# Kernel optimization log

Hardware: AMD Instinct MI355X
Metric: run time of the kernel (lower is better)

The kernel has to match this reference:

```python
import jax, jax.numpy as jnp
import numpy as np

DIM = 96
GS = 8          # group_size (window side)
CS = 64         # cluster_size
TOPK = 3


def setup_inputs() -> dict:
    key = jax.random.key(0)
    ks = jax.random.split(key, 12)
    B, C, H, W = 4, DIM, 256, 256
    s = 0.02
    return {
        "x":      jax.random.normal(ks[0], (B, C, H, W), jnp.float32),
        "Wq":     jax.random.normal(ks[1], (C, C), jnp.float32) * s,
        "bq":     jnp.zeros((C,), jnp.float32),
        "Wk":     jax.random.normal(ks[2], (C, C), jnp.float32) * s,
        "bk":     jnp.zeros((C,), jnp.float32),
        "Wv":     jax.random.normal(ks[3], (C, C), jnp.float32) * s,
        "bv":     jnp.zeros((C,), jnp.float32),
        "Wp":     jax.random.normal(ks[4], (C, C), jnp.float32) * s,
        "bp":     jnp.zeros((C,), jnp.float32),
        "lepe_w": jax.random.normal(ks[5], (C, 1, 3, 3), jnp.float32) * s,
        "lepe_b": jnp.zeros((C,), jnp.float32),
    }


def _dwconv3x3(x, w, b):
    # x: [N,C,h,w], w: [C,1,3,3] depthwise
    y = jax.lax.conv_general_dilated(
        x, w, window_strides=(1, 1), padding=((1, 1), (1, 1)),
        feature_group_count=x.shape[1],
        dimension_numbers=("NCHW", "OIHW", "NCHW"))
    return y + b[None, :, None, None]


def reference(x, Wq, bq, Wk, bk, Wv, bv, Wp, bp, lepe_w, lepe_b):
    B, C, H, W = x.shape
    gh, gw = H // GS, W // GS
    N = B * gh * gw                      # total windows
    itr = N // CS                        # number of clusters
    P = GS * GS                          # tokens per window
    scale = C ** (-0.5)

    # adaptive_max_pool2d to (gh,gw) == non-overlapping max pool of stride GS
    dsx = x.reshape(B, C, gh, GS, gw, GS).max(axis=(3, 5))        # [B,C,gh,gw]
    dsx = dsx.transpose(0, 2, 3, 1).reshape(itr, CS, C)           # [itr,CS,C]

    # global window-similarity with two-stage topk (faithful to nested loop)
    sim = jnp.einsum('icd,jed->icje', dsx, dsx)                   # [itr,CS,itr,CS]
    blk_s, blk_i = jax.lax.top_k(sim, TOPK)                       # [itr,CS,itr,TOPK]
    blk_gi = blk_i + (jnp.arange(itr) * CS)[None, None, :, None]  # global indices
    cat_s = blk_s.reshape(itr, CS, itr * TOPK)
    cat_i = blk_gi.reshape(itr, CS, itr * TOPK)
    fin_s, fi = jax.lax.top_k(cat_s, TOPK)                        # [itr,CS,TOPK]
    fin_i = jnp.take_along_axis(cat_i, fi, axis=-1)
    sim_score = fin_s.reshape(N, TOPK)
    sim_index = fin_i.reshape(N, TOPK)

    # window partition: [N, P, C]
    xw = x.transpose(0, 2, 3, 1).reshape(B, gh, GS, gw, GS, C)
    xw = xw.transpose(0, 1, 3, 2, 4, 5).reshape(N, P, C)

    # weighted combination of topk neighbor windows
    w = jax.nn.softmax(sim_score, axis=-1)                        # [N,TOPK]
    neighbors = xw[sim_index]                                     # [N,TOPK,P,C]
    context = jnp.einsum('nk,nkpc->npc', w, neighbors)            # [N,P,C]

    # windowed cross attention: Q from x windows, K/V from gathered context
    q = xw @ Wq + bq
    k = context @ Wk + bk
    v = context @ Wv + bv

    # lepe: depthwise conv positional bias on x windows
    x_img = xw.transpose(0, 2, 1).reshape(N, C, GS, GS)
    lepe = _dwconv3x3(x_img, lepe_w, lepe_b).reshape(N, C, P).transpose(0, 2, 1)

    attn = jax.nn.softmax(jnp.einsum('npc,nqc->npq', q, k) * scale, axis=-1)
    out = jnp.einsum('npq,nqc->npc', attn, v) + lepe
    out = out @ Wp + bp                                           # [N,P,C]

    # reverse window partition -> [B,C,H,W]
    out = out.reshape(B, gh, gw, GS, GS, C)
    out = out.transpose(0, 5, 1, 3, 2, 4).reshape(B, C, H, W)
    return out
```

## Files before the change

kernel.cpp:

```cpp
#include <hip/hip_runtime.h>

typedef __attribute__((ext_vector_type(8))) short  short8;
typedef __attribute__((ext_vector_type(4))) float  f32x4;
typedef __attribute__((ext_vector_type(4))) unsigned int uint4v;
typedef __attribute__((ext_vector_type(2))) unsigned int uint2v;

#define NEG_INF (-3.402823466e38f)

__device__ __forceinline__ unsigned short bfbits(float f) {
    unsigned u = __builtin_bit_cast(unsigned, f);
    u += 0x7fffu + ((u >> 16) & 1u);
    return (unsigned short)(u >> 16);
}
__device__ __forceinline__ unsigned pk_bf16(float lo, float hi) {
    return (unsigned)bfbits(lo) | ((unsigned)bfbits(hi) << 16);
}
__device__ __forceinline__ float lofp(unsigned u) {
    return __builtin_bit_cast(float, u << 16);
}
__device__ __forceinline__ float hifp(unsigned u) {
    return __builtin_bit_cast(float, u & 0xffff0000u);
}

__device__ __forceinline__ void ins3(float (&tv)[3], int (&ti)[3], float v, int ci)
{
    if (v > tv[0] || (v == tv[0] && ci < ti[0])) {
        tv[2] = tv[1]; ti[2] = ti[1];
        tv[1] = tv[0]; ti[1] = ti[0];
        tv[0] = v;     ti[0] = ci;
    } else if (v > tv[1] || (v == tv[1] && ci < ti[1])) {
        tv[2] = tv[1]; ti[2] = ti[1];
        tv[1] = v;     ti[1] = ci;
    } else if (v > tv[2] || (v == tv[2] && ci < ti[2])) {
        tv[2] = v;     ti[2] = ci;
    }
}

__global__ __launch_bounds__(256) void k_pool(const float* __restrict__ x,
                                              float* __restrict__ dsxT)
{
    int gid = blockIdx.x * 256 + threadIdx.x;
    int c = gid >> 12;
    int n = gid & 4095;
    int b = n >> 10, i = (n >> 5) & 31, j = n & 31;
    const float* p = x + (((size_t)(b * 96 + c)) << 16) + i * 2048 + j * 8;
    float4 m0 = *(const float4*)p;
    float4 m1 = *(const float4*)(p + 4);
    #pragma unroll
    for (int r = 1; r < 8; ++r) {
        float4 a0 = *(const float4*)(p + r * 256);
        float4 a1 = *(const float4*)(p + r * 256 + 4);
        m0.x = fmaxf(m0.x, a0.x); m0.y = fmaxf(m0.y, a0.y);
        m0.z = fmaxf(m0.z, a0.z); m0.w = fmaxf(m0.w, a0.w);
        m1.x = fmaxf(m1.x, a1.x); m1.y = fmaxf(m1.y, a1.y);
        m1.z = fmaxf(m1.z, a1.z); m1.w = fmaxf(m1.w, a1.w);
    }
    float m = fmaxf(fmaxf(fmaxf(m0.x, m0.y), fmaxf(m0.z, m0.w)),
                    fmaxf(fmaxf(m1.x, m1.y), fmaxf(m1.z, m1.w)));
    dsxT[c * 4096 + n] = m;
}

__global__ __launch_bounds__(768) void k_cast(const float* __restrict__ x,
                                              unsigned short* __restrict__ xwg,
                                              float* __restrict__ dsxT)
{
    int n = blockIdx.x;
    int t = threadIdx.x;
    int cg = t >> 6, p = t & 63;
    int b = n >> 10, i = (n >> 5) & 31, j = n & 31;
    int h = i * 8 + (p >> 3), w = j * 8 + (p & 7);
    size_t base = (((size_t)(b * 96 + 8 * cg)) << 16) + (size_t)(h * 256 + w);
    float v[8];
    #pragma unroll
    for (int jj = 0; jj < 8; ++jj) v[jj] = x[base + (((size_t)jj) << 16)];
    uint4v pk;
    #pragma unroll
    for (int jj = 0; jj < 4; ++jj) pk[jj] = pk_bf16(v[2 * jj], v[2 * jj + 1]);
    *(uint4v*)&xwg[(size_t)n * 6144 + p * 96 + 8 * cg] = pk;
    #pragma unroll
    for (int jj = 0; jj < 8; ++jj) {
        float m = v[jj];
        #pragma unroll
        for (int d = 1; d < 64; d <<= 1) m = fmaxf(m, __shfl_xor(m, d, 64));
        if (p == 0) dsxT[(8 * cg + jj) * 4096 + n] = m;
    }
}

__global__ __launch_bounds__(256) void k_sim(const float* __restrict__ dsxT,
                                             float* __restrict__ pv,
                                             int* __restrict__ pi)
{
    __shared__ __align__(16) float qt[32 * 128];
    __shared__ __align__(16) float ct[32 * 144];
    int t = threadIdx.x;
    int qti = blockIdx.x >> 4;
    int ch  = blockIdx.x & 15;
    int ty = t >> 4, tx = t & 15;
    int qb = qti * 128;

    float tv[8][3]; int ti[8][3];
    #pragma unroll
    for (int a = 0; a < 8; ++a)
        #pragma unroll
        for (int k = 0; k < 3; ++k) { tv[a][k] = NEG_INF; ti[a][k] = 0x7fffffff; }

    #pragma unroll
    for (int pass = 0; pass < 2; ++pass) {
        int cb = ch * 256 + pass * 128;
        float acc[8][8];
        #pragma unroll
        for (int a = 0; a < 8; ++a)
            #pragma unroll
            for (int e = 0; e < 8; ++e) acc[a][e] = 0.f;

        for (int kc = 0; kc < 3; ++kc) {
            __syncthreads();
            #pragma unroll
            for (int f4 = 0; f4 < 4; ++f4) {
                int f = t + f4 * 256;
                int kk = f >> 5, cq = f & 31;
                *(float4*)&qt[kk * 128 + 4 * cq] =
                    *(const float4*)&dsxT[(kc * 32 + kk) * 4096 + qb + 4 * cq];
                *(float4*)&ct[kk * 144 + 4 * cq + 4 * (cq >> 3)] =
                    *(const float4*)&dsxT[(kc * 32 + kk) * 4096 + cb + 4 * cq];
            }
            __syncthreads();
            #pragma unroll 2
            for (int kk = 0; kk < 32; ++kk) {
                float4 q0 = *(float4*)&qt[kk * 128 + 8 * ty];
                float4 q1 = *(float4*)&qt[kk * 128 + 8 * ty + 4];
                int e0 = 8 * tx, e1 = 8 * tx + 4;
                float4 c0 = *(float4*)&ct[kk * 144 + e0 + 4 * (e0 >> 5)];
                float4 c1 = *(float4*)&ct[kk * 144 + e1 + 4 * (e1 >> 5)];
                float qv[8] = {q0.x, q0.y, q0.z, q0.w, q1.x, q1.y, q1.z, q1.w};
                float cv[8] = {c0.x, c0.y, c0.z, c0.w, c1.x, c1.y, c1.z, c1.w};
                #pragma unroll
                for (int a = 0; a < 8; ++a)
                    #pragma unroll
                    for (int e = 0; e < 8; ++e)
                        acc[a][e] = fmaf(qv[a], cv[e], acc[a][e]);
            }
        }
        #pragma unroll
        for (int e = 0; e < 8; ++e) {
            int ci = cb + 8 * tx + e;
            #pragma unroll
            for (int a = 0; a < 8; ++a) ins3(tv[a], ti[a], acc[a][e], ci);
        }
    }

    #pragma unroll
    for (int d = 1; d < 16; d <<= 1) {
        #pragma unroll
        for (int a = 0; a < 8; ++a) {
            float ov[3]; int oi[3];
            #pragma unroll
            for (int k = 0; k < 3; ++k) {
                ov[k] = __shfl_xor(tv[a][k], d, 16);
                oi[k] = __shfl_xor(ti[a][k], d, 16);
            }
            #pragma unroll
            for (int k = 0; k < 3; ++k) ins3(tv[a], ti[a], ov[k], oi[k]);
        }
    }
    if (tx == 0) {
        #pragma unroll
        for (int a = 0; a < 8; ++a) {
            int nq = qti * 128 + 8 * ty + a;
            #pragma unroll
            for (int k = 0; k < 3; ++k) {
                pv[nq * 48 + ch * 3 + k] = tv[a][k];
                pi[nq * 48 + ch * 3 + k] = ti[a][k];
            }
        }
    }
}

__global__ __launch_bounds__(256) void k_topk(const float* __restrict__ pv,
                                              const int* __restrict__ pi,
                                              float* __restrict__ w3,
                                              int* __restrict__ i3)
{
    int n = blockIdx.x * 256 + threadIdx.x;
    float bv[3] = {NEG_INF, NEG_INF, NEG_INF};
    int   bi[3] = {0x7fffffff, 0x7fffffff, 0x7fffffff};
    for (int e = 0; e < 48; ++e)
        ins3(bv, bi, pv[n * 48 + e], pi[n * 48 + e]);
    float e1 = expf(bv[1] - bv[0]);
    float e2 = expf(bv[2] - bv[0]);
    float inv = 1.f / (1.f + e1 + e2);
    w3[n * 3 + 0] = inv;
    w3[n * 3 + 1] = e1 * inv;
    w3[n * 3 + 2] = e2 * inv;
    i3[n * 3 + 0] = bi[0];
    i3[n * 3 + 1] = bi[1];
    i3[n * 3 + 2] = bi[2];
}

__global__ __launch_bounds__(256) void k_prep(const float* __restrict__ Wq,
                                              const float* __restrict__ Wk,
                                              const float* __restrict__ Wv,
                                              const float* __restrict__ Wp,
                                              const float* __restrict__ lw,
                                              unsigned short* __restrict__ WtT,
                                              float* __restrict__ lwT)
{
    int g = blockIdx.x * 256 + threadIdx.x;
    if (g < 4608) {
        int w  = g / 1152;
        int co = (g % 1152) / 12;
        int cg = g % 12;
        const float* src = (w == 0) ? Wq : (w == 1) ? Wk : (w == 2) ? Wv : Wp;
        unsigned short* dst = WtT + w * 9216 + co * 96 + 8 * cg;
        #pragma unroll
        for (int j = 0; j < 8; ++j) dst[j] = bfbits(src[(8 * cg + j) * 96 + co]);
    } else if (g < 5472) {
        int i2 = g - 4608;
        int tap = i2 / 96, c = i2 % 96;
        lwT[tap * 96 + c] = lw[c * 9 + tap];
    }
}

__device__ __forceinline__ size_t win_off(int m)
{
    return (((size_t)(m >> 10) * 96) << 16) +
           (size_t)(((m >> 5) & 31) * 2048 + (m & 31) * 8);
}

__device__ __forceinline__ void gemm_g(const short8* af,
                                       const unsigned short* __restrict__ Wt,
                                       int l15, int quad, f32x4* acc)
{
    #pragma unroll
    for (int nt = 0; nt < 6; ++nt) {
        f32x4 c = {0.f, 0.f, 0.f, 0.f};
        #pragma unroll
        for (int ks = 0; ks < 3; ++ks) {
            short8 bf = *(const short8*)&Wt[(nt * 16 + l15) * 96 + ks * 32 + quad * 8];
            c = __builtin_amdgcn_mfma_f32_16x16x32_bf16(af[ks], bf, c, 0, 0, 0);
        }
        acc[nt] = c;
    }
}

template<bool XWG>
__global__ __attribute__((amdgpu_waves_per_eu(4, 4)))
__launch_bounds__(256) void k_attn(
    const float* __restrict__ x,
    const unsigned short* __restrict__ xwg,
    const unsigned short* __restrict__ WtT,
    const float* __restrict__ lwT,
    const float* __restrict__ bq, const float* __restrict__ bk,
    const float* __restrict__ bv, const float* __restrict__ bp,
    const float* __restrict__ lb,
    const float* __restrict__ w3, const int* __restrict__ i3,
    float* __restrict__ out)
{
    extern __shared__ __align__(16) unsigned short sm[];
    unsigned short* buf1 = sm;
    unsigned short* buf2 = sm + 6656;
    unsigned short* Vt   = sm + 13312;

    int t = threadIdx.x;
    int n = blockIdx.x;
    int lane = t & 63, mt = t >> 6;
    int l15 = lane & 15, quad = lane >> 4;

    float wk0 = w3[n * 3 + 0], wk1 = w3[n * 3 + 1], wk2 = w3[n * 3 + 2];
    int   m0  = i3[n * 3 + 0], m1 = i3[n * 3 + 1], m2 = i3[n * 3 + 2];

    if (XWG) {
        #pragma unroll
        for (int it = 0; it < 3; ++it) {
            int g = it * 256 + t;
            int p = g / 12, cg = g % 12;
            int o = p * 96 + 8 * cg;
            uint4v sv = *(const uint4v*)&xwg[(size_t)n * 6144 + o];
            *(uint4v*)&buf1[p * 104 + 8 * cg] = sv;
            uint4v a0 = *(const uint4v*)&xwg[(size_t)m0 * 6144 + o];
            uint4v a1 = *(const uint4v*)&xwg[(size_t)m1 * 6144 + o];
            uint4v a2 = *(const uint4v*)&xwg[(size_t)m2 * 6144 + o];
            uint4v rs;
            #pragma unroll
            for (int e = 0; e < 4; ++e) {
                float lo = wk0 * lofp(a0[e]) + wk1 * lofp(a1[e]) + wk2 * lofp(a2[e]);
                float hi = wk0 * hifp(a0[e]) + wk1 * hifp(a1[e]) + wk2 * hifp(a2[e]);
                rs[e] = pk_bf16(lo, hi);
            }
            *(uint4v*)&buf2[p * 104 + 8 * cg] = rs;
        }
    } else {
        size_t so = win_off(n), o0 = win_off(m0), o1 = win_off(m1), o2 = win_off(m2);
        #pragma unroll
        for (int it = 0; it < 3; ++it) {
            int g = it * 256 + t;
            int p = g / 12, cg = g % 12;
            size_t po = (size_t)((p >> 3) * 256 + (p & 7));
            uint4v ra, rb;
            #pragma unroll
            for (int jj = 0; jj < 4; ++jj) {
                size_t clo = (((size_t)(8 * cg + 2 * jj)) << 16) + po;
                size_t chi = clo + ((size_t)1 << 16);
                ra[jj] = pk_bf16(x[so + clo], x[so + chi]);
                float blo = wk0 * x[o0 + clo] + wk1 * x[o1 + clo] + wk2 * x[o2 + clo];
                float bhi = wk0 * x[o0 + chi] + wk1 * x[o1 + chi] + wk2 * x[o2 + chi];
                rb[jj] = pk_bf16(blo, bhi);
            }
            *(uint4v*)&buf1[p * 104 + 8 * cg] = ra;
            *(uint4v*)&buf2[p * 104 + 8 * cg] = rb;
        }
    }
    __syncthreads();

    short8 af_a[3], af_b[3];
    int arow = (mt * 16 + l15) * 104;
    #pragma unroll
    for (int ks = 0; ks < 3; ++ks) {
        af_a[ks] = *(const short8*)&buf1[arow + ks * 32 + quad * 8];
        af_b[ks] = *(const short8*)&buf2[arow + ks * 32 + quad * 8];
    }
    unsigned Lp[12];
    {
        int rowp = mt * 16 + l15;
        int c0 = 24 * quad;
        int rr0 = rowp >> 3, ss0 = rowp & 7;
        float lac[24];
        #pragma unroll
        for (int q4 = 0; q4 < 6; ++q4) {
            float4 bb = *(const float4*)&lb[c0 + 4 * q4];
            lac[4 * q4] = bb.x; lac[4 * q4 + 1] = bb.y;
            lac[4 * q4 + 2] = bb.z; lac[4 * q4 + 3] = bb.w;
        }
        #pragma unroll
        for (int dr = -1; dr <= 1; ++dr) {
            int rr = rr0 + dr;
            if ((unsigned)rr >= 8u) continue;
            #pragma unroll
            for (int dss = -1; dss <= 1; ++dss) {
                int ss = ss0 + dss;
                if ((unsigned)ss >= 8u) continue;
                int pp = rr * 8 + ss;
                int tap = (dr + 1) * 3 + (dss + 1);
                const uint4v* ap = (const uint4v*)&buf1[pp * 104 + c0];
                uint4v av0 = ap[0], av1 = ap[1], av2 = ap[2];
                float wf[24];
                #pragma unroll
                for (int q4 = 0; q4 < 6; ++q4) {
                    float4 ww = *(const float4*)&lwT[tap * 96 + c0 + 4 * q4];
                    wf[4 * q4] = ww.x; wf[4 * q4 + 1] = ww.y;
                    wf[4 * q4 + 2] = ww.z; wf[4 * q4 + 3] = ww.w;
                }
                #pragma unroll
                for (int u = 0; u < 12; ++u) {
                    unsigned uu = (u < 4) ? av0[u] : (u < 8) ? av1[u - 4] : av2[u - 8];
                    lac[2 * u]     = fmaf(wf[2 * u],     lofp(uu), lac[2 * u]);
                    lac[2 * u + 1] = fmaf(wf[2 * u + 1], hifp(uu), lac[2 * u + 1]);
                }
            }
        }
        #pragma unroll
        for (int u = 0; u < 12; ++u) Lp[u] = pk_bf16(lac[2 * u], lac[2 * u + 1]);
    }
    __syncthreads();

    {
        f32x4 qa[6];
        gemm_g(af_a, WtT, l15, quad, qa);
        #pragma unroll
        for (int nt = 0; nt < 6; ++nt) {
            int col = nt * 16 + l15;
            float bb = bq[col];
            #pragma unroll
            for (int r = 0; r < 4; ++r)
                buf1[(mt * 16 + quad * 4 + r) * 104 + col] = bfbits(qa[nt][r] + bb);
        }
    }
    __builtin_amdgcn_sched_barrier(0);
    {
        f32x4 ka[6];
        gemm_g(af_b, WtT + 9216, l15, quad, ka);
        #pragma unroll
        for (int nt = 0; nt < 6; ++nt) {
            int col = nt * 16 + l15;
            float bb = bk[col];
            #pragma unroll
            for (int r = 0; r < 4; ++r)
                buf2[(mt * 16 + quad * 4 + r) * 104 + col] = bfbits(ka[nt][r] + bb);
        }
    }
    __builtin_amdgcn_sched_barrier(0);
    {
        f32x4 va[6];
        gemm_g(af_b, WtT + 18432, l15, quad, va);
        #pragma unroll
        for (int nt = 0; nt < 6; ++nt) {
            float bb = bv[nt * 16 + l15];
            uint2v pk;
            pk[0] = pk_bf16(va[nt][0] + bb, va[nt][1] + bb);
            pk[1] = pk_bf16(va[nt][2] + bb, va[nt][3] + bb);
            *(uint2v*)&Vt[(nt * 16 + l15) * 72 + mt * 16 + quad * 4] = pk;
        }
    }
    __syncthreads();

    float pr[4][4], inv4[4];
    {
        short8 qf[3];
        #pragma unroll
        for (int ks = 0; ks < 3; ++ks)
            qf[ks] = *(const short8*)&buf1[arow + ks * 32 + quad * 8];
        f32x4 sa[4];
        #pragma unroll
        for (int nt = 0; nt < 4; ++nt) {
            f32x4 c = {0.f, 0.f, 0.f, 0.f};
            #pragma unroll
            for (int ks = 0; ks < 3; ++ks) {
                short8 bf = *(const short8*)&buf2[(nt * 16 + l15) * 104 + ks * 32 + quad * 8];
                c = __builtin_amdgcn_mfma_f32_16x16x32_bf16(qf[ks], bf, c, 0, 0, 0);
            }
            sa[nt] = c;
        }
        const float scale = 0.10206207261596575f;
        #pragma unroll
        for (int r = 0; r < 4; ++r) {
            float mx = fmaxf(fmaxf(sa[0][r], sa[1][r]), fmaxf(sa[2][r], sa[3][r]));
            #pragma unroll
            for (int d = 1; d < 16; d <<= 1) mx = fmaxf(mx, __shfl_xor(mx, d, 16));
            float sum = 0.f;
            #pragma unroll
            for (int nt = 0; nt < 4; ++nt) {
                float e = __expf((sa[nt][r] - mx) * scale);
                pr[r][nt] = e; sum += e;
            }
            #pragma unroll
            for (int d = 1; d < 16; d <<= 1) sum += __shfl_xor(sum, d, 16);
            inv4[r] = 1.f / sum;
        }
    }
    __syncthreads();

    #pragma unroll
    for (int r = 0; r < 4; ++r) {
        #pragma unroll
        for (int nt = 0; nt < 4; ++nt)
            buf1[(mt * 16 + quad * 4 + r) * 104 + nt * 16 + l15] =
                bfbits(pr[r][nt] * inv4[r]);
    }
    {
        uint4v* lp = (uint4v*)&buf2[arow + 24 * quad];
        uint4v l0 = {Lp[0], Lp[1], Lp[2], Lp[3]};
        uint4v l1 = {Lp[4], Lp[5], Lp[6], Lp[7]};
        uint4v l2 = {Lp[8], Lp[9], Lp[10], Lp[11]};
        lp[0] = l0; lp[1] = l1; lp[2] = l2;
    }

    {
        short8 sf[2];
        sf[0] = *(const short8*)&buf1[arow + quad * 8];
        sf[1] = *(const short8*)&buf1[arow + 32 + quad * 8];
        f32x4 oa[6];
        #pragma unroll
        for (int nt = 0; nt < 6; ++nt) {
            f32x4 c = {0.f, 0.f, 0.f, 0.f};
            #pragma unroll
            for (int ks = 0; ks < 2; ++ks) {
                short8 bf = *(const short8*)&Vt[(nt * 16 + l15) * 72 + ks * 32 + quad * 8];
                c = __builtin_amdgcn_mfma_f32_16x16x32_bf16(sf[ks], bf, c, 0, 0, 0);
            }
            oa[nt] = c;
        }
        #pragma unroll
        for (int nt = 0; nt < 6; ++nt)
            #pragma unroll
            for (int r = 0; r < 4; ++r)
                buf1[(mt * 16 + quad * 4 + r) * 104 + nt * 16 + l15] = bfbits(oa[nt][r]);
    }

    {
        short8 of[3], lf[3];
        #pragma unroll
        for (int ks = 0; ks < 3; ++ks) {
            of[ks] = *(const short8*)&buf1[arow + ks * 32 + quad * 8];
            lf[ks] = *(const short8*)&buf2[arow + ks * 32 + quad * 8];
        }
        const unsigned short* Wp_ = WtT + 27648;
        int b = n >> 10, ii = (n >> 5) & 31, jj = n & 31;
        size_t pbase = (size_t)(ii * 2048 + jj * 8 + mt * 512 +
                                (quad >> 1) * 256 + (quad & 1) * 4);
        #pragma unroll
        for (int nt = 0; nt < 6; ++nt) {
            f32x4 c = {0.f, 0.f, 0.f, 0.f};
            #pragma unroll
            for (int ks = 0; ks < 3; ++ks) {
                short8 bf = *(const short8*)&Wp_[(nt * 16 + l15) * 96 + ks * 32 + quad * 8];
                c = __builtin_amdgcn_mfma_f32_16x16x32_bf16(of[ks], bf, c, 0, 0, 0);
                c = __builtin_amdgcn_mfma_f32_16x16x32_bf16(lf[ks], bf, c, 0, 0, 0);
            }
            int co = nt * 16 + l15;
            float bb = bp[co];
            float4 st;
            st.x = c[0] + bb; st.y = c[1] + bb; st.z = c[2] + bb; st.w = c[3] + bb;
            *(float4*)&out[(((size_t)(b * 96 + co)) << 16) + pbase] = st;
        }
    }
}

extern "C" void kernel_launch(void* const* d_in, const int* in_sizes, int n_in,
                              void* d_out, int out_size, void* d_ws, size_t ws_size,
                              hipStream_t stream)
{
    (void)in_sizes; (void)n_in; (void)out_size;
    const float* x  = (const float*)d_in[0];
    const float* Wq = (const float*)d_in[1];
    const float* bq = (const float*)d_in[2];
    const float* Wk = (const float*)d_in[3];
    const float* bk = (const float*)d_in[4];
    const float* Wv = (const float*)d_in[5];
    const float* bv = (const float*)d_in[6];
    const float* Wp = (const float*)d_in[7];
    const float* bp = (const float*)d_in[8];
    const float* lw = (const float*)d_in[9];
    const float* lb = (const float*)d_in[10];
    float* out = (float*)d_out;

    char* ws = (char*)d_ws;
    float* dsxT = (float*)ws;
    float* pv   = (float*)(ws + 1572864);
    int*   pi   = (int*)  (ws + 2359296);
    float* w3   = (float*)(ws + 3145728);
    int*   i3   = (int*)  (ws + 3194880);
    unsigned short* WtT = (unsigned short*)(ws + 3244032);
    float* lwT  = (float*)(ws + 3317760);
    unsigned short* xwg = (unsigned short*)(ws + 3321344);
    bool use_xwg = (ws_size >= 53652992ull);

    (void)hipFuncSetAttribute(reinterpret_cast<const void*>(&k_attn<true>),
                        hipFuncAttributeMaxDynamicSharedMemorySize, 40448);
    (void)hipFuncSetAttribute(reinterpret_cast<const void*>(&k_attn<false>),
                        hipFuncAttributeMaxDynamicSharedMemorySize, 40448);

    k_prep<<<22, 256, 0, stream>>>(Wq, Wk, Wv, Wp, lw, WtT, lwT);
    if (use_xwg) {
        k_cast<<<4096, 768, 0, stream>>>(x, xwg, dsxT);
    } else {
        k_pool<<<1536, 256, 0, stream>>>(x, dsxT);
    }
    k_sim<<<512, 256, 0, stream>>>(dsxT, pv, pi);
    k_topk<<<16, 256, 0, stream>>>(pv, pi, w3, i3);
    if (use_xwg) {
        k_attn<true><<<4096, 256, 40448, stream>>>(x, xwg, WtT, lwT, bq, bk, bv, bp,
                                                   lb, w3, i3, out);
    } else {
        k_attn<false><<<4096, 256, 40448, stream>>>(x, nullptr, WtT, lwT, bq, bk, bv, bp,
                                                    lb, w3, i3, out);
    }
}
```

Measured before the change: 449.1 us.

## Compute window similarity with split-bf16 MFMA and exact fp32 rescoring of candidates

The pooled window descriptors are stored as three bf16 parts (high, mid, low), and the 4096x4096 similarity search runs on bf16 MFMA using six partial products, replacing the fp32 scalar path. A new kernel then rescores each window's 48 candidates exactly in fp32, picks the top-3 with wave shuffles and computes the softmax weights, replacing the serial per-thread top-k. Block indices in k_cast and k_attn are also remapped to interleave windows across batches. The split-bf16 product is only approximate, so the first-stage per-chunk selection can differ from the fp32 reference when similarities are nearly tied.

Result: faster. 428.4 us (-4.6%).

```diff
diff --git a/kernel.cpp b/kernel.cpp
--- a/kernel.cpp
+++ b/kernel.cpp
@@ -20,6 +20,9 @@
 }
 __device__ __forceinline__ float hifp(unsigned u) {
     return __builtin_bit_cast(float, u & 0xffff0000u);
+}
+__device__ __forceinline__ float bf2f(short x) {
+    return __builtin_bit_cast(float, ((unsigned)(unsigned short)x) << 16);
 }
 
 __device__ __forceinline__ void ins3(float (&tv)[3], int (&ti)[3], float v, int ci)
@@ -62,9 +65,11 @@
 
 __global__ __launch_bounds__(768) void k_cast(const float* __restrict__ x,
                                               unsigned short* __restrict__ xwg,
-                                              float* __restrict__ dsxT)
-{
-    int n = blockIdx.x;
+                                              unsigned short* __restrict__ dsxH,
+                                              unsigned short* __restrict__ dsxM,
+                                              unsigned short* __restrict__ dsxL)
+{
+    int n = ((blockIdx.x & 7) << 9) | (blockIdx.x >> 3);
     int t = threadIdx.x;
     int cg = t >> 6, p = t & 63;
     int b = n >> 10, i = (n >> 5) & 31, j = n & 31;
@@ -82,7 +87,15 @@
         float m = v[jj];
         #pragma unroll
         for (int d = 1; d < 64; d <<= 1) m = fmaxf(m, __shfl_xor(m, d, 64));
-        if (p == 0) dsxT[(8 * cg + jj) * 4096 + n] = m;
+        if (p == 0) {
+            unsigned short hb = bfbits(m);
+            float r1 = m - __builtin_bit_cast(float, ((unsigned)hb) << 16);
+            unsigned short mb = bfbits(r1);
+            float r2 = r1 - __builtin_bit_cast(float, ((unsigned)mb) << 16);
+            dsxH[n * 96 + 8 * cg + jj] = hb;
+            dsxM[n * 96 + 8 * cg + jj] = mb;
+            dsxL[n * 96 + 8 * cg + jj] = bfbits(r2);
+        }
     }
 }
 
@@ -176,6 +189,135 @@
     }
 }
 
+__global__ __launch_bounds__(256) void k_sim_bf(const unsigned short* __restrict__ dsxH,
+                                                const unsigned short* __restrict__ dsxM,
+                                                const unsigned short* __restrict__ dsxL,
+                                                int* __restrict__ pi)
+{
+    int t = threadIdx.x;
+    int qti = blockIdx.x >> 4;
+    int ch  = blockIdx.x & 15;
+    int lane = t & 63, wv = t >> 6;
+    int l15 = lane & 15, quad = lane >> 4;
+    int cb = ch * 256;
+
+    #pragma unroll
+    for (int a2 = 0; a2 < 2; ++a2) {
+        int at = wv * 2 + a2;
+        int qrow = qti * 128 + at * 16 + l15;
+        short8 aH[3], aM[3], aL[3];
+        #pragma unroll
+        for (int ks = 0; ks < 3; ++ks) {
+            aH[ks] = *(const short8*)&dsxH[qrow * 96 + ks * 32 + quad * 8];
+            aM[ks] = *(const short8*)&dsxM[qrow * 96 + ks * 32 + quad * 8];
+            aL[ks] = *(const short8*)&dsxL[qrow * 96 + ks * 32 + quad * 8];
+        }
+        float tv[4][3]; int ti[4][3];
+        #pragma unroll
+        for (int r = 0; r < 4; ++r)
+            #pragma unroll
+            for (int k = 0; k < 3; ++k) { tv[r][k] = NEG_INF; ti[r][k] = 0x7fffffff; }
+
+        for (int bt = 0; bt < 16; ++bt) {
+            int crow = cb + bt * 16 + l15;
+            f32x4 c  = {0.f, 0.f, 0.f, 0.f};
+            f32x4 c2 = {0.f, 0.f, 0.f, 0.f};
+            #pragma unroll
+            for (int ks = 0; ks < 3; ++ks) {
+                short8 bH = *(const short8*)&dsxH[crow * 96 + ks * 32 + quad * 8];
+                short8 bM = *(const short8*)&dsxM[crow * 96 + ks * 32 + quad * 8];
+                short8 bL = *(const short8*)&dsxL[crow * 96 + ks * 32 + quad * 8];
+                c  = __builtin_amdgcn_mfma_f32_16x16x32_bf16(aH[ks], bH, c,  0, 0, 0);
+                c2 = __builtin_amdgcn_mfma_f32_16x16x32_bf16(aH[ks], bM, c2, 0, 0, 0);
+                c2 = __builtin_amdgcn_mfma_f32_16x16x32_bf16(aM[ks], bH, c2, 0, 0, 0);
+                c2 = __builtin_amdgcn_mfma_f32_16x16x32_bf16(aM[ks], bM, c2, 0, 0, 0);
+                c2 = __builtin_amdgcn_mfma_f32_16x16x32_bf16(aH[ks], bL, c2, 0, 0, 0);
+                c2 = __builtin_amdgcn_mfma_f32_16x16x32_bf16(aL[ks], bH, c2, 0, 0, 0);
+            }
+            #pragma unroll
+            for (int r = 0; r < 4; ++r)
+                ins3(tv[r], ti[r], c[r] + c2[r], cb + bt * 16 + l15);
+        }
+        #pragma unroll
+        for (int d = 1; d < 16; d <<= 1) {
+            #pragma unroll
+            for (int r = 0; r < 4; ++r) {
+                float ov[3]; int oi[3];
+                #pragma unroll
+                for (int k = 0; k < 3; ++k) {
+                    ov[k] = __shfl_xor(tv[r][k], d, 16);
+                    oi[k] = __shfl_xor(ti[r][k], d, 16);
+                }
+                #pragma unroll
+                for (int k = 0; k < 3; ++k) ins3(tv[r], ti[r], ov[k], oi[k]);
+            }
+        }
+        if (l15 == 0) {
+            #pragma unroll
+            for (int r = 0; r < 4; ++r) {
+                int nq = qti * 128 + at * 16 + quad * 4 + r;
+                #pragma unroll
+                for (int k = 0; k < 3; ++k)
+                    pi[nq * 48 + ch * 3 + k] = ti[r][k];
+            }
+        }
+    }
+}
+
+__global__ __launch_bounds__(256) void k_top3x(const unsigned short* __restrict__ dsxH,
+                                               const unsigned short* __restrict__ dsxM,
+                                               const unsigned short* __restrict__ dsxL,
+                                               const int* __restrict__ pi,
+                                               float* __restrict__ w3,
+                                               int* __restrict__ i3)
+{
+    int t = threadIdx.x;
+    int lane = t & 63, wv = t >> 6;
+    int n = blockIdx.x * 4 + wv;
+    int cand = (lane < 48) ? pi[n * 48 + lane] : 0;
+    float s = 0.f;
+    #pragma unroll
+    for (int ck = 0; ck < 12; ++ck) {
+        short8 qh = *(const short8*)&dsxH[n * 96 + ck * 8];
+        short8 qm = *(const short8*)&dsxM[n * 96 + ck * 8];
+        short8 ql = *(const short8*)&dsxL[n * 96 + ck * 8];
+        short8 kh = *(const short8*)&dsxH[cand * 96 + ck * 8];
+        short8 km = *(const short8*)&dsxM[cand * 96 + ck * 8];
+        short8 kl = *(const short8*)&dsxL[cand * 96 + ck * 8];
+        #pragma unroll
+        for (int e = 0; e < 8; ++e) {
+            float qv = (bf2f(qh[e]) + bf2f(qm[e])) + bf2f(ql[e]);
+            float kv = (bf2f(kh[e]) + bf2f(km[e])) + bf2f(kl[e]);
+            s = fmaf(qv, kv, s);
+        }
+    }
+    float tv[3] = {NEG_INF, NEG_INF, NEG_INF};
+    int   ti[3] = {0x7fffffff, 0x7fffffff, 0x7fffffff};
+    if (lane < 48) { tv[0] = s; ti[0] = cand; }
+    #pragma unroll
+    for (int d = 1; d < 64; d <<= 1) {
+        float ov[3]; int oi[3];
+        #pragma unroll
+        for (int k = 0; k < 3; ++k) {
+            ov[k] = __shfl_xor(tv[k], d, 64);
+            oi[k] = __shfl_xor(ti[k], d, 64);
+        }
+        #pragma unroll
+        for (int k = 0; k < 3; ++k) ins3(tv, ti, ov[k], oi[k]);
+    }
+    if (lane == 0) {
+        float e1 = expf(tv[1] - tv[0]);
+        float e2 = expf(tv[2] - tv[0]);
+        float inv = 1.f / (1.f + e1 + e2);
+        w3[n * 3 + 0] = inv;
+        w3[n * 3 + 1] = e1 * inv;
+        w3[n * 3 + 2] = e2 * inv;
+        i3[n * 3 + 0] = ti[0];
+        i3[n * 3 + 1] = ti[1];
+        i3[n * 3 + 2] = ti[2];
+    }
+}
+
 __global__ __launch_bounds__(256) void k_topk(const float* __restrict__ pv,
                                               const int* __restrict__ pi,
                                               float* __restrict__ w3,
@@ -262,7 +404,7 @@
     unsigned short* Vt   = sm + 13312;
 
     int t = threadIdx.x;
-    int n = blockIdx.x;
+    int n = ((blockIdx.x & 7) << 9) | (blockIdx.x >> 3);
     int lane = t & 63, mt = t >> 6;
     int l15 = lane & 15, quad = lane >> 4;
 
@@ -525,6 +667,9 @@
 
     char* ws = (char*)d_ws;
     float* dsxT = (float*)ws;
+    unsigned short* dsxH = (unsigned short*)ws;
+    unsigned short* dsxM = (unsigned short*)(ws + 786432);
+    unsigned short* dsxL = (unsigned short*)(ws + 1572864);
     float* pv   = (float*)(ws + 1572864);
     int*   pi   = (int*)  (ws + 2359296);
     float* w3   = (float*)(ws + 3145728);
@@ -541,16 +686,15 @@
 
     k_prep<<<22, 256, 0, stream>>>(Wq, Wk, Wv, Wp, lw, WtT, lwT);
     if (use_xwg) {
-        k_cast<<<4096, 768, 0, stream>>>(x, xwg, dsxT);
-    } else {
-        k_pool<<<1536, 256, 0, stream>>>(x, dsxT);
-    }
-    k_sim<<<512, 256, 0, stream>>>(dsxT, pv, pi);
-    k_topk<<<16, 256, 0, stream>>>(pv, pi, w3, i3);
-    if (use_xwg) {
+        k_cast<<<4096, 768, 0, stream>>>(x, xwg, dsxH, dsxM, dsxL);
+        k_sim_bf<<<512, 256, 0, stream>>>(dsxH, dsxM, dsxL, pi);
+        k_top3x<<<1024, 256, 0, stream>>>(dsxH, dsxM, dsxL, pi, w3, i3);
         k_attn<true><<<4096, 256, 40448, stream>>>(x, xwg, WtT, lwT, bq, bk, bv, bp,
                                                    lb, w3, i3, out);
     } else {
+        k_pool<<<1536, 256, 0, stream>>>(x, dsxT);
+        k_sim<<<512, 256, 0, stream>>>(dsxT, pv, pi);
+        k_topk<<<16, 256, 0, stream>>>(pv, pi, w3, i3);
         k_attn<false><<<4096, 256, 40448, stream>>>(x, nullptr, WtT, lwT, bq, bk, bv, bp,
                                                     lb, w3, i3, out);
     }
```
